# Kernel tuning notes

Measured on AMD Instinct MI355X. Metric: run time of the kernel, lower is better.

The kernel has to match this reference:

```python
import jax, jax.numpy as jnp
import numpy as np

B = 32768
N_PATCH = 196  # 14x14 grid of 2x2 patches over a 28x28 image
DIM = 16       # 2^4 state-vector dimension for 4 wires


def setup_inputs() -> dict:
    key = jax.random.key(0)
    kx, = jax.random.split(key, 1)
    # pixel data in [0,1] like normalized MNIST
    x = jax.random.uniform(kx, (B, 784), dtype=jnp.float32)
    # fixed random 2-qubit layer composed into a single real orthogonal 16x16 unitary
    rng = np.random.default_rng(0)
    q, _ = np.linalg.qr(rng.standard_normal((DIM, DIM)))
    U = jnp.asarray(q, dtype=jnp.float32)
    return {"x": x, "U": U}


def _pauli_z_signs():
    # Z[w, b] = +1 if bit w of basis index b is 0 else -1 (wire 0 = MSB, kron order)
    wires = jnp.arange(4)[:, None]
    basis = jnp.arange(DIM)[None, :]
    bits = (basis >> (3 - wires)) & 1
    return 1.0 - 2.0 * bits.astype(jnp.float32)  # [4, 16]


def reference(x, U):
    bsz = x.shape[0]
    img = x.reshape(bsz, 28, 28)
    # extract 2x2 patches in the same row-major order as the original loop:
    # data = [x[r,c], x[r,c+1], x[r+1,c], x[r+1,c+1]] -> [B, 196, 4]
    data = img.reshape(bsz, 14, 2, 14, 2).transpose(0, 1, 3, 2, 4).reshape(bsz, N_PATCH, 4)
    # RY(theta)|0> = cos(theta/2)|0> + sin(theta/2)|1> per wire (real amplitudes)
    half = 0.5 * data
    q = jnp.stack([jnp.cos(half), jnp.sin(half)], axis=-1)  # [B, 196, 4, 2]
    # product state via kron over the 4 wires -> [B, 196, 16]
    state = jnp.einsum('bpi,bpj,bpk,bpl->bpijkl',
                       q[:, :, 0], q[:, :, 1], q[:, :, 2], q[:, :, 3]
                       ).reshape(bsz, N_PATCH, DIM)
    # apply the fixed random layer unitary
    state = jnp.einsum('bpd,ed->bpe', state, U)
    # PauliZ expectation on each wire from |amp|^2
    probs = state * state
    Z = _pauli_z_signs()  # [4, 16]
    meas = jnp.einsum('bpd,wd->bpw', probs, Z)  # [B, 196, 4]
    return meas.reshape(bsz, N_PATCH * 4)
```

## Files before the change

kernel.cpp:

```cpp
#include <hip/hip_runtime.h>

typedef _Float16 half4 __attribute__((ext_vector_type(4)));
typedef _Float16 h2 __attribute__((ext_vector_type(2)));
typedef float f32x4 __attribute__((ext_vector_type(4)));

#define SINCONST 0.07957747154594767f

__device__ __forceinline__ unsigned int pk(float a, float b) {
    return __builtin_bit_cast(unsigned int, __builtin_amdgcn_cvt_pkrtz(a, b));
}

__device__ __forceinline__ void factors(float px0, float px1, float px2, float px3,
                                        uint2& aw, uint2& qw) {
    float t0 = px0 * SINCONST, t1 = px1 * SINCONST;
    float t2 = px2 * SINCONST, t3 = px3 * SINCONST;
    float s0 = __builtin_amdgcn_sinf(t0), c0 = __builtin_amdgcn_cosf(t0);
    float s1 = __builtin_amdgcn_sinf(t1), c1 = __builtin_amdgcn_cosf(t1);
    float s2 = __builtin_amdgcn_sinf(t2), c2 = __builtin_amdgcn_cosf(t2);
    float s3 = __builtin_amdgcn_sinf(t3), c3 = __builtin_amdgcn_cosf(t3);
    float a0 = c0 * c1, a1 = c0 * s1, a2 = s0 * c1, a3 = s0 * s1;
    float q0 = c2 * c3, q1 = c2 * s3, q2 = s2 * c3, q3 = s2 * s3;
    aw.x = pk(a0, a1); aw.y = pk(a2, a3);
    qw.x = pk(q0, q1); qw.y = pk(q2, q3);
}

__global__ __launch_bounds__(256, 7) void quanv(
    const float* __restrict__ x,
    const float* __restrict__ U,
    float* __restrict__ out,
    int total, int ipw, int rem)
{
    __shared__ __align__(16) unsigned int smem[4 * 1024];

    const int tid  = threadIdx.x;
    const int lane = tid & 63;
    const int wib  = tid >> 6;
    const int wave = (blockIdx.x * 256 + tid) >> 6;
    const int p16  = lane & 15;
    const int g    = lane >> 4;

    unsigned int* wbase = smem + wib * 1024;

    half4 aU;
    {
        const float* up = U + p16 * 16 + 4 * g;
        aU[0] = (_Float16)up[0];
        aU[1] = (_Float16)up[1];
        aU[2] = (_Float16)up[2];
        aU[3] = (_Float16)up[3];
    }
    half4 aS;
    {
        int w = p16 & 3;
        #pragma unroll
        for (int i = 0; i < 4; ++i) {
            int e = 4 * g + i;
            aS[i] = ((e >> (3 - w)) & 1) ? (_Float16)-1.f : (_Float16)1.f;
        }
    }

    int cnt = ipw + (wave < rem ? 1 : 0);
    if (cnt <= 0) return;
    const int mac0 = wave * ipw + (wave < rem ? wave : rem);
    const int nPairs = total >> 1;

    auto ldp = [&](int j, float4& t4, float4& b4) {
        int PR = (mac0 + j) * 64 + lane;
        if (PR >= nPairs) PR = nPairs - 1;
        int P   = PR * 2;
        int img = P / 196;
        int pp  = P - img * 196;
        int r   = (pp * 2341) >> 15;
        const float4* ptr = reinterpret_cast<const float4*>(x + img * 784 + 2 * pp + 28 * r);
        t4 = ptr[0];
        b4 = ptr[7];
    };

    auto do_factors = [&](int jj, float4 T, float4 Bt) {
        unsigned int* buf = wbase + (jj & 1) * 512;
        uint2 awA, qwA, awB, qwB;
        factors(T.x, T.y, Bt.x, Bt.y, awA, qwA);
        factors(T.z, T.w, Bt.z, Bt.w, awB, qwB);
        *reinterpret_cast<uint4*>(buf + lane * 4)       = make_uint4(awA.x, awA.y, awB.x, awB.y);
        *reinterpret_cast<uint4*>(buf + 256 + lane * 4) = make_uint4(qwA.x, qwA.y, qwB.x, qwB.y);
    };

    float4 cT, cB, fT, fB;
    ldp(0, cT, cB);
    ldp(1, fT, fB);
    do_factors(0, cT, cB);

    for (int j = 0; j < cnt; ++j) {
        cT = fT; cB = fB;
        ldp(j + 2, fT, fB);

        do_factors(j + 1, cT, cB);

        const unsigned int* buf2 = wbase + (j & 1) * 512;
        const unsigned short* ap = reinterpret_cast<const unsigned short*>(buf2);
        const int pbase = (mac0 + j) * 128;

        #pragma unroll
        for (int th = 0; th < 2; ++th) {
            f32x4 mm[4];
            #pragma unroll
            for (int i = 0; i < 4; ++i) {
                const int t  = th * 4 + i;
                const int pt = t * 16 + p16;
                unsigned int av = ap[pt * 4 + g];
                unsigned int dup = (av << 16) | av;
                uint2 qw = *reinterpret_cast<const uint2*>(buf2 + 256 + pt * 2);

                h2 ag  = __builtin_bit_cast(h2, dup);
                h2 q01 = __builtin_bit_cast(h2, qw.x);
                h2 q23 = __builtin_bit_cast(h2, qw.y);
                h2 blo = ag * q01;
                h2 bhi = ag * q23;
                half4 bST = __builtin_shufflevector(blo, bhi, 0, 1, 2, 3);

                const f32x4 zero4 = {0.f, 0.f, 0.f, 0.f};
                f32x4 y = __builtin_amdgcn_mfma_f32_16x16x16f16(aU, bST, zero4, 0, 0, 0);

                h2 y01 = __builtin_bit_cast(h2, pk(y[0], y[1]));
                h2 y23 = __builtin_bit_cast(h2, pk(y[2], y[3]));
                h2 p01 = y01 * y01;
                h2 p23 = y23 * y23;
                half4 bP = __builtin_shufflevector(p01, p23, 0, 1, 2, 3);

                mm[i] = __builtin_amdgcn_mfma_f32_16x16x16f16(aS, bP, zero4, 0, 0, 0);
            }
            f32x4 sa  = (g & 1) ? mm[1] : mm[0];
            f32x4 sb  = (g & 1) ? mm[3] : mm[2];
            f32x4 sel = (g & 2) ? sb : sa;
            int Ps = pbase + th * 64 + lane;
            if (Ps < total)
                __builtin_nontemporal_store(sel, reinterpret_cast<f32x4*>(out + (size_t)Ps * 4));
        }
    }
}

extern "C" void kernel_launch(void* const* d_in, const int* in_sizes, int n_in,
                              void* d_out, int out_size, void* d_ws, size_t ws_size,
                              hipStream_t stream) {
    const float* x = (const float*)d_in[0];
    const float* U = (const float*)d_in[1];
    float* out = (float*)d_out;

    int B = in_sizes[0] / 784;
    int total = B * 196;
    int nPairs = total / 2;
    int nmac = (nPairs + 63) / 64;

    int nblocks = 1792;
    int nwaves = nblocks * (256 / 64);
    int ipw = nmac / nwaves;
    int rem = nmac % nwaves;

    quanv<<<nblocks, 256, 0, stream>>>(x, U, out, total, ipw, rem);
}
```

Baseline: 41.00 us.

## Stage contiguous half-image chunks in LDS with coalesced loads, one chunk per iteration

Each wave now loads a contiguous 448-float chunk (half an image, 112 patches) with fully coalesced uint4 loads into LDS, then gathers the 2x2 patches from LDS instead of issuing scattered per-lane global float4 loads that need div/mod addressing. The work split changes to a fixed 7 chunks per wave with a grid sized to match, replacing the ipw/rem distribution and the tail bounds checks. Patch batches drop from 8 to 7 MFMA groups per chunk, so some lanes sit idle in the final group. Only compiler fences order the per-wave LDS accesses, which depends on wave-level lockstep, and the fixed launch_bounds occupancy hint is removed.

```diff
diff --git a/kernel.cpp b/kernel.cpp
--- a/kernel.cpp
+++ b/kernel.cpp
@@ -6,8 +6,14 @@
 
 #define SINCONST 0.07957747154594767f
 
+#define CFENCE() asm volatile("" ::: "memory")
+
 __device__ __forceinline__ unsigned int pk(float a, float b) {
     return __builtin_bit_cast(unsigned int, __builtin_amdgcn_cvt_pkrtz(a, b));
+}
+
+__device__ __forceinline__ float uf(unsigned int u) {
+    return __builtin_bit_cast(float, u);
 }
 
 __device__ __forceinline__ void factors(float px0, float px1, float px2, float px3,
@@ -24,13 +30,13 @@
     qw.x = pk(q0, q1); qw.y = pk(q2, q3);
 }
 
-__global__ __launch_bounds__(256, 7) void quanv(
+__global__ __launch_bounds__(256) void quanv(
     const float* __restrict__ x,
     const float* __restrict__ U,
     float* __restrict__ out,
-    int total, int ipw, int rem)
+    int nchunks)
 {
-    __shared__ __align__(16) unsigned int smem[4 * 1024];
+    __shared__ __align__(16) unsigned int smem[4 * 896];
 
     const int tid  = threadIdx.x;
     const int lane = tid & 63;
@@ -39,7 +45,7 @@
     const int p16  = lane & 15;
     const int g    = lane >> 4;
 
-    unsigned int* wbase = smem + wib * 1024;
+    unsigned int* wl = smem + wib * 896;
 
     half4 aU;
     {
@@ -59,83 +65,106 @@
         }
     }
 
-    int cnt = ipw + (wave < rem ? 1 : 0);
+    const int ch0 = wave * 7;
+    int cnt = nchunks - ch0;
     if (cnt <= 0) return;
-    const int mac0 = wave * ipw + (wave < rem ? wave : rem);
-    const int nPairs = total >> 1;
+    if (cnt > 7) cnt = 7;
 
-    auto ldp = [&](int j, float4& t4, float4& b4) {
-        int PR = (mac0 + j) * 64 + lane;
-        if (PR >= nPairs) PR = nPairs - 1;
-        int P   = PR * 2;
-        int img = P / 196;
-        int pp  = P - img * 196;
-        int r   = (pp * 2341) >> 15;
-        const float4* ptr = reinterpret_cast<const float4*>(x + img * 784 + 2 * pp + 28 * r);
-        t4 = ptr[0];
-        b4 = ptr[7];
-    };
+    const uint4* xu = reinterpret_cast<const uint4*>(x);
 
-    auto do_factors = [&](int jj, float4 T, float4 Bt) {
-        unsigned int* buf = wbase + (jj & 1) * 512;
-        uint2 awA, qwA, awB, qwB;
-        factors(T.x, T.y, Bt.x, Bt.y, awA, qwA);
-        factors(T.z, T.w, Bt.z, Bt.w, awB, qwB);
-        *reinterpret_cast<uint4*>(buf + lane * 4)       = make_uint4(awA.x, awA.y, awB.x, awB.y);
-        *reinterpret_cast<uint4*>(buf + 256 + lane * 4) = make_uint4(qwA.x, qwA.y, qwB.x, qwB.y);
-    };
-
-    float4 cT, cB, fT, fB;
-    ldp(0, cT, cB);
-    ldp(1, fT, fB);
-    do_factors(0, cT, cB);
+    uint4 v0, v1;
+    {
+        const uint4* src = xu + (size_t)ch0 * 112;
+        v0 = src[lane];
+        if (lane < 48) v1 = src[64 + lane];
+    }
+    *reinterpret_cast<uint4*>(wl + 4 * lane) = v0;
+    if (lane < 48) *reinterpret_cast<uint4*>(wl + 256 + 4 * lane) = v1;
+    CFENCE();
 
     for (int j = 0; j < cnt; ++j) {
-        cT = fT; cB = fB;
-        ldp(j + 2, fT, fB);
+        const int ch = ch0 + j;
 
-        do_factors(j + 1, cT, cB);
+        if (j + 1 < cnt) {
+            const uint4* src = xu + (size_t)(ch + 1) * 112;
+            v0 = src[lane];
+            if (lane < 48) v1 = src[64 + lane];
+        }
 
-        const unsigned int* buf2 = wbase + (j & 1) * 512;
-        const unsigned short* ap = reinterpret_cast<const unsigned short*>(buf2);
-        const int pbase = (mac0 + j) * 128;
+        {
+            const int p = lane;
+            int rp = (p * 2341) >> 15;
+            int base = 2 * p + 28 * rp;
+            uint2 t2 = *reinterpret_cast<const uint2*>(wl + base);
+            uint2 b2 = *reinterpret_cast<const uint2*>(wl + base + 28);
+            uint2 aw, qw;
+            factors(uf(t2.x), uf(t2.y), uf(b2.x), uf(b2.y), aw, qw);
+            *reinterpret_cast<uint2*>(wl + 448 + 2 * p) = aw;
+            *reinterpret_cast<uint2*>(wl + 672 + 2 * p) = qw;
+        }
+        if (lane < 48) {
+            const int p = 64 + lane;
+            int rp = (p * 2341) >> 15;
+            int base = 2 * p + 28 * rp;
+            uint2 t2 = *reinterpret_cast<const uint2*>(wl + base);
+            uint2 b2 = *reinterpret_cast<const uint2*>(wl + base + 28);
+            uint2 aw, qw;
+            factors(uf(t2.x), uf(t2.y), uf(b2.x), uf(b2.y), aw, qw);
+            *reinterpret_cast<uint2*>(wl + 448 + 2 * p) = aw;
+            *reinterpret_cast<uint2*>(wl + 672 + 2 * p) = qw;
+        }
+        CFENCE();
 
-        #pragma unroll
-        for (int th = 0; th < 2; ++th) {
-            f32x4 mm[4];
-            #pragma unroll
-            for (int i = 0; i < 4; ++i) {
-                const int t  = th * 4 + i;
-                const int pt = t * 16 + p16;
-                unsigned int av = ap[pt * 4 + g];
-                unsigned int dup = (av << 16) | av;
-                uint2 qw = *reinterpret_cast<const uint2*>(buf2 + 256 + pt * 2);
+        const unsigned short* ap = reinterpret_cast<const unsigned short*>(wl + 448);
+        const int pbase = ch * 112;
+        f32x4* out4 = reinterpret_cast<f32x4*>(out);
 
-                h2 ag  = __builtin_bit_cast(h2, dup);
-                h2 q01 = __builtin_bit_cast(h2, qw.x);
-                h2 q23 = __builtin_bit_cast(h2, qw.y);
-                h2 blo = ag * q01;
-                h2 bhi = ag * q23;
-                half4 bST = __builtin_shufflevector(blo, bhi, 0, 1, 2, 3);
+        auto batch = [&](int t) -> f32x4 {
+            const int pt = t * 16 + p16;
+            unsigned int av = ap[pt * 4 + g];
+            unsigned int dup = (av << 16) | av;
+            uint2 qw = *reinterpret_cast<const uint2*>(wl + 672 + 2 * pt);
 
-                const f32x4 zero4 = {0.f, 0.f, 0.f, 0.f};
-                f32x4 y = __builtin_amdgcn_mfma_f32_16x16x16f16(aU, bST, zero4, 0, 0, 0);
+            h2 ag  = __builtin_bit_cast(h2, dup);
+            h2 q01 = __builtin_bit_cast(h2, qw.x);
+            h2 q23 = __builtin_bit_cast(h2, qw.y);
+            h2 blo = ag * q01;
+            h2 bhi = ag * q23;
+            half4 bST = __builtin_shufflevector(blo, bhi, 0, 1, 2, 3);
 
-                h2 y01 = __builtin_bit_cast(h2, pk(y[0], y[1]));
-                h2 y23 = __builtin_bit_cast(h2, pk(y[2], y[3]));
-                h2 p01 = y01 * y01;
-                h2 p23 = y23 * y23;
-                half4 bP = __builtin_shufflevector(p01, p23, 0, 1, 2, 3);
+            const f32x4 zero4 = {0.f, 0.f, 0.f, 0.f};
+            f32x4 y = __builtin_amdgcn_mfma_f32_16x16x16f16(aU, bST, zero4, 0, 0, 0);
 
-                mm[i] = __builtin_amdgcn_mfma_f32_16x16x16f16(aS, bP, zero4, 0, 0, 0);
-            }
-            f32x4 sa  = (g & 1) ? mm[1] : mm[0];
-            f32x4 sb  = (g & 1) ? mm[3] : mm[2];
+            h2 y01 = __builtin_bit_cast(h2, pk(y[0], y[1]));
+            h2 y23 = __builtin_bit_cast(h2, pk(y[2], y[3]));
+            h2 p01 = y01 * y01;
+            h2 p23 = y23 * y23;
+            half4 bP = __builtin_shufflevector(p01, p23, 0, 1, 2, 3);
+
+            return __builtin_amdgcn_mfma_f32_16x16x16f16(aS, bP, zero4, 0, 0, 0);
+        };
+
+        {
+            f32x4 m0 = batch(0), m1 = batch(1), m2 = batch(2), m3 = batch(3);
+            f32x4 sa  = (g & 1) ? m1 : m0;
+            f32x4 sb  = (g & 1) ? m3 : m2;
             f32x4 sel = (g & 2) ? sb : sa;
-            int Ps = pbase + th * 64 + lane;
-            if (Ps < total)
-                __builtin_nontemporal_store(sel, reinterpret_cast<f32x4*>(out + (size_t)Ps * 4));
+            __builtin_nontemporal_store(sel, out4 + pbase + lane);
         }
+        {
+            f32x4 m0 = batch(4), m1 = batch(5), m2 = batch(6);
+            f32x4 sel = (g & 1) ? m1 : m0;
+            sel = (g & 2) ? m2 : sel;
+            if (lane < 48)
+                __builtin_nontemporal_store(sel, out4 + pbase + 64 + lane);
+        }
+        CFENCE();
+
+        if (j + 1 < cnt) {
+            *reinterpret_cast<uint4*>(wl + 4 * lane) = v0;
+            if (lane < 48) *reinterpret_cast<uint4*>(wl + 256 + 4 * lane) = v1;
+        }
+        CFENCE();
     }
 }
 
@@ -147,14 +176,9 @@
     float* out = (float*)d_out;
 
     int B = in_sizes[0] / 784;
-    int total = B * 196;
-    int nPairs = total / 2;
-    int nmac = (nPairs + 63) / 64;
+    int nchunks = (B * 784) / 448;
+    int nwaves = (nchunks + 6) / 7;
+    int nblocks = (nwaves + 3) / 4;
 
-    int nblocks = 1792;
-    int nwaves = nblocks * (256 / 64);
-    int ipw = nmac / nwaves;
-    int rem = nmac % nwaves;
-
-    quanv<<<nblocks, 256, 0, stream>>>(x, U, out, total, ipw, rem);
+    quanv<<<nblocks, 256, 0, stream>>>(x, U, out, nchunks);
 }
```

Result: no change. 40.34 us (-1.6%).
